# Kernel optimization log

Measured on AMD Instinct MI355X. Metric: run time of the kernel, lower is better.

## Reference

```python
import jax, jax.numpy as jnp
import numpy as np


def _conv1x1(x, w, b):
    # x: (B,C_in,H,W), w: (C_out,C_in), b: (C_out,)
    return jnp.einsum('bchw,oc->bohw', x, w) + b[None, :, None, None]


def _maxpool2x2(x):
    B, C, H, W = x.shape
    return x.reshape(B, C, H // 2, 2, W // 2, 2).max(axis=(3, 5))


def setup_inputs() -> dict:
    key = jax.random.key(0)
    ks = jax.random.split(key, 10)
    B, C, H, W = 16, 64, 64, 64
    d8, d2 = C // 8, C // 2
    s = 0.05
    return {
        'x': jax.random.normal(ks[0], (B, C, H, W), dtype=jnp.float32),
        'w_theta': jax.random.normal(ks[1], (d8, C), dtype=jnp.float32) * s,
        'b_theta': jnp.zeros((d8,), dtype=jnp.float32),
        'w_phi': jax.random.normal(ks[2], (d8, C), dtype=jnp.float32) * s,
        'b_phi': jnp.zeros((d8,), dtype=jnp.float32),
        'w_g': jax.random.normal(ks[3], (d2, C), dtype=jnp.float32) * s,
        'b_g': jnp.zeros((d2,), dtype=jnp.float32),
        'w_o': jax.random.normal(ks[4], (C, d2), dtype=jnp.float32) * s,
        'b_o': jnp.zeros((C,), dtype=jnp.float32),
        'sigma': jnp.ones((1,), dtype=jnp.float32),
    }


def reference(x, w_theta, b_theta, w_phi, b_phi, w_g, b_g, w_o, b_o, sigma):
    B, C, H, W = x.shape
    N = H * W
    theta = _conv1x1(x, w_theta, b_theta).reshape(B, C // 8, N)            # (B, d8, N)
    phi = _maxpool2x2(_conv1x1(x, w_phi, b_phi)).reshape(B, C // 8, N // 4)  # (B, d8, N/4)
    attn = jax.nn.softmax(jnp.einsum('bdn,bdm->bnm', theta, phi), axis=-1)   # (B, N, N/4)
    g = _maxpool2x2(_conv1x1(x, w_g, b_g)).reshape(B, C // 2, N // 4)        # (B, d2, N/4)
    attn_g = jnp.einsum('bcm,bnm->bcn', g, attn).reshape(B, C // 2, H, W)
    attn_g = _conv1x1(attn_g, w_o, b_o)
    return x + sigma[0] * attn_g
```

## Files before the change

kernel.cpp:

```cpp
#include <hip/hip_runtime.h>


#define B_   16
#define C_   64
#define HW_  4096
#define M_   1024

typedef __attribute__((ext_vector_type(8))) short bf16x8;
typedef __attribute__((ext_vector_type(4))) float f32x4;

__device__ __forceinline__ unsigned short f2bf(float f) {
    union { float f; unsigned int u; } v; v.f = f;
    return (unsigned short)((v.u + 0x7FFFu + ((v.u >> 16) & 1u)) >> 16);
}
__device__ __forceinline__ unsigned int pack2(float a, float b) {
    return (unsigned int)f2bf(a) | ((unsigned int)f2bf(b) << 16);
}

__global__ __launch_bounds__(256) void proj_kernel(
    const float* __restrict__ x,
    const float* __restrict__ w_theta, const float* __restrict__ b_theta,
    const float* __restrict__ w_phi,   const float* __restrict__ b_phi,
    const float* __restrict__ w_g,     const float* __restrict__ b_g,
    unsigned short* __restrict__ thetaB,
    unsigned short* __restrict__ phiB32,
    unsigned short* __restrict__ gTp)
{
    __shared__ __align__(16) float x_l[64 * 132];
    __shared__ float pool_l[128][41];

    const int tid = threadIdx.x;
    const int b   = blockIdx.y;
    const int rp  = blockIdx.x;
    const int n0  = rp * 128;

    {
        const float4* src = (const float4*)(x + (size_t)b * C_ * HW_ + n0);
        #pragma unroll
        for (int j = 0; j < 8; j++) {
            int idx = tid + j * 256;
            int c = idx >> 5, p4 = idx & 31;
            float4 v = src[(size_t)c * (HW_ / 4) + p4];
            *(float4*)&x_l[c * 132 + p4 * 4] = v;
        }
    }
    __syncthreads();

    const int px = tid & 127;
    const int og = tid >> 7;

    if (og == 0) {
        float th[8], ph[8], g0[8];
        #pragma unroll
        for (int o = 0; o < 8; o++) { th[o] = b_theta[o]; ph[o] = b_phi[o]; g0[o] = b_g[o]; }
        #pragma unroll 4
        for (int c = 0; c < C_; c++) {
            float xv = x_l[c * 132 + px];
            #pragma unroll
            for (int o = 0; o < 8; o++) th[o] += xv * w_theta[o * 64 + c];
            #pragma unroll
            for (int o = 0; o < 8; o++) ph[o] += xv * w_phi[o * 64 + c];
            #pragma unroll
            for (int o = 0; o < 8; o++) g0[o] += xv * w_g[o * 64 + c];
        }
        unsigned short* tout = thetaB + ((size_t)b * HW_ + n0 + px) * 8;
        uint4 tv;
        tv.x = pack2(th[0], th[1]); tv.y = pack2(th[2], th[3]);
        tv.z = pack2(th[4], th[5]); tv.w = pack2(th[6], th[7]);
        *(uint4*)tout = tv;
        #pragma unroll
        for (int o = 0; o < 8; o++) { pool_l[px][o] = ph[o]; pool_l[px][8 + o] = g0[o]; }
    } else {
        float gg[24];
        #pragma unroll
        for (int o = 0; o < 24; o++) gg[o] = b_g[8 + o];
        #pragma unroll 4
        for (int c = 0; c < C_; c++) {
            float xv = x_l[c * 132 + px];
            #pragma unroll
            for (int o = 0; o < 24; o++) gg[o] += xv * w_g[(8 + o) * 64 + c];
        }
        #pragma unroll
        for (int o = 0; o < 24; o++) pool_l[px][16 + o] = gg[o];
    }
    __syncthreads();

    if (tid < 32) {
        const int pc  = tid;
        const int p00 = 2 * pc, p01 = 2 * pc + 1, p10 = 64 + 2 * pc, p11 = 65 + 2 * pc;
        const int mq  = rp * 32 + pc;
        float o8[8];
        #pragma unroll
        for (int o = 0; o < 8; o++)
            o8[o] = fmaxf(fmaxf(pool_l[p00][o], pool_l[p01][o]),
                          fmaxf(pool_l[p10][o], pool_l[p11][o]));
        unsigned short* pout = phiB32 + ((size_t)b * M_ + mq) * 32;
        uint4 pv;
        pv.x = pack2(o8[0], o8[1]); pv.y = pack2(o8[2], o8[3]);
        pv.z = pack2(o8[4], o8[5]); pv.w = pack2(o8[6], o8[7]);
        ((uint4*)pout)[0] = pv;
        ((uint4*)pout)[1] = make_uint4(0, 0, 0, 0);
        ((uint4*)pout)[2] = make_uint4(0, 0, 0, 0);
        ((uint4*)pout)[3] = make_uint4(0, 0, 0, 0);
    } else if (tid < 64) {
        const int j   = tid - 32;
        const int p00 = 2 * j, p01 = 2 * j + 1, p10 = 64 + 2 * j, p11 = 65 + 2 * j;
        const int pcol = rp * 32 + ((j >> 2) & 3) * 8 + (j >> 4) * 4 + (j & 3);
        unsigned short* gout = gTp + (size_t)b * 32 * M_ + pcol;
        #pragma unroll
        for (int c = 0; c < 32; c++) {
            const int s = c + 8;
            float v = fmaxf(fmaxf(pool_l[p00][s], pool_l[p01][s]),
                            fmaxf(pool_l[p10][s], pool_l[p11][s]));
            gout[(size_t)c * M_] = f2bf(v);
        }
    }
}

__global__ __launch_bounds__(256) void attn_kernel(
    const float* __restrict__ x,
    const unsigned short* __restrict__ thetaB,
    const unsigned short* __restrict__ phiB32,
    const unsigned short* __restrict__ gTp,
    const float* __restrict__ w_o, const float* __restrict__ b_o,
    const float* __restrict__ sigma,
    float* __restrict__ out)
{
    __shared__ float Op_l[4][64 * 33];
    __shared__ float rs_l[4][64];

    const int tid   = threadIdx.x;
    const int b     = blockIdx.y;
    const int qbase = blockIdx.x * 64;
    const int wv    = tid >> 6;
    const int lane  = tid & 63;
    const int ln15  = lane & 15;
    const int quad  = lane >> 4;

    const unsigned short* phiP = phiB32 + (size_t)b * M_ * 32;
    const unsigned short* gP   = gTp    + (size_t)b * 32 * M_;

    bf16x8 th[4];
    {
        const bf16x8 z = {0, 0, 0, 0, 0, 0, 0, 0};
        #pragma unroll
        for (int qt = 0; qt < 4; qt++) {
            const unsigned short* tp =
                thetaB + ((size_t)b * HW_ + qbase + qt * 16 + ln15) * 8;
            bf16x8 t = *(const bf16x8*)tp;
            th[qt] = (quad == 0) ? t : z;
        }
    }

    #define LD_PHI(ch_, mt_) \
        (*(const bf16x8*)(phiP + ((size_t)((ch_) * 64 + (mt_) * 16 + ln15)) * 32 + quad * 8))
    #define LD_G(ch_, h_, s_) \
        (*(const bf16x8*)(gP + (size_t)((h_) * 16 + ln15) * M_ + (ch_) * 64 + (s_) * 32 + quad * 8))

    f32x4 acc[2][4];
    #pragma unroll
    for (int h = 0; h < 2; h++)
        #pragma unroll
        for (int qt = 0; qt < 4; qt++) acc[h][qt] = (f32x4){0.f, 0.f, 0.f, 0.f};
    float rs_p[4] = {0.f, 0.f, 0.f, 0.f};

    bf16x8 pf[4], gf[2][2];
    {
        const int ch = wv * 4;
        #pragma unroll
        for (int mt = 0; mt < 4; mt++) pf[mt] = LD_PHI(ch, mt);
        gf[0][0] = LD_G(ch, 0, 0); gf[0][1] = LD_G(ch, 0, 1);
        gf[1][0] = LD_G(ch, 1, 0); gf[1][1] = LD_G(ch, 1, 1);
    }

    for (int wc = 0; wc < 4; wc++) {
        const int nch = wv * 4 + ((wc < 3) ? wc + 1 : 3);
        bf16x8 npf[4], ngf[2][2];
        #pragma unroll
        for (int mt = 0; mt < 4; mt++) npf[mt] = LD_PHI(nch, mt);
        ngf[0][0] = LD_G(nch, 0, 0); ngf[0][1] = LD_G(nch, 0, 1);
        ngf[1][0] = LD_G(nch, 1, 0); ngf[1][1] = LD_G(nch, 1, 1);

        #pragma unroll
        for (int s = 0; s < 2; s++) {
            #pragma unroll
            for (int qt = 0; qt < 4; qt++) {
                const f32x4 zc = {0.f, 0.f, 0.f, 0.f};
                f32x4 S0 = __builtin_amdgcn_mfma_f32_16x16x32_bf16(pf[2 * s],     th[qt], zc, 0, 0, 0);
                f32x4 S1 = __builtin_amdgcn_mfma_f32_16x16x32_bf16(pf[2 * s + 1], th[qt], zc, 0, 0, 0);
                float e0[4], e1[4];
                #pragma unroll
                for (int r = 0; r < 4; r++) {
                    e0[r] = __expf(S0[r]);
                    e1[r] = __expf(S1[r]);
                    rs_p[qt] += e0[r] + e1[r];
                }
                union { bf16x8 v; unsigned int u[4]; } pb;
                pb.u[0] = pack2(e0[0], e0[1]); pb.u[1] = pack2(e0[2], e0[3]);
                pb.u[2] = pack2(e1[0], e1[1]); pb.u[3] = pack2(e1[2], e1[3]);
                acc[0][qt] = __builtin_amdgcn_mfma_f32_16x16x32_bf16(gf[0][s], pb.v, acc[0][qt], 0, 0, 0);
                acc[1][qt] = __builtin_amdgcn_mfma_f32_16x16x32_bf16(gf[1][s], pb.v, acc[1][qt], 0, 0, 0);
            }
        }

        #pragma unroll
        for (int mt = 0; mt < 4; mt++) pf[mt] = npf[mt];
        gf[0][0] = ngf[0][0]; gf[0][1] = ngf[0][1];
        gf[1][0] = ngf[1][0]; gf[1][1] = ngf[1][1];
    }
    #undef LD_PHI
    #undef LD_G

    {
        float v[4];
        #pragma unroll
        for (int qt = 0; qt < 4; qt++) {
            float t = rs_p[qt];
            t += __shfl_xor(t, 16);
            t += __shfl_xor(t, 32);
            v[qt] = t;
        }
        if (quad == 0) {
            #pragma unroll
            for (int qt = 0; qt < 4; qt++) rs_l[wv][qt * 16 + ln15] = v[qt];
        }
    }
    #pragma unroll
    for (int h = 0; h < 2; h++)
        #pragma unroll
        for (int qt = 0; qt < 4; qt++)
            #pragma unroll
            for (int r = 0; r < 4; r++)
                Op_l[wv][(qt * 16 + ln15) * 33 + h * 16 + quad * 4 + r] = acc[h][qt][r];
    __syncthreads();

    const int q = tid & 63;
    const float rowsum = rs_l[0][q] + rs_l[1][q] + rs_l[2][q] + rs_l[3][q];
    const float sg  = sigma[0];
    const float inv = sg / rowsum;
    float o[32];
    #pragma unroll
    for (int c = 0; c < 32; c++)
        o[c] = Op_l[0][q * 33 + c] + Op_l[1][q * 33 + c]
             + Op_l[2][q * 33 + c] + Op_l[3][q * 33 + c];
    const size_t xb = (size_t)b * C_ * HW_ + qbase + q;
    #pragma unroll
    for (int k = 0; k < 16; k++) {
        const int co = wv * 16 + k;
        float t = 0.f;
        #pragma unroll
        for (int c = 0; c < 32; c++) t += w_o[co * 32 + c] * o[c];
        out[xb + (size_t)co * HW_] = x[xb + (size_t)co * HW_] + t * inv + sg * b_o[co];
    }
}

extern "C" void kernel_launch(void* const* d_in, const int* in_sizes, int n_in,
                              void* d_out, int out_size, void* d_ws, size_t ws_size,
                              hipStream_t stream)
{
    const float* x       = (const float*)d_in[0];
    const float* w_theta = (const float*)d_in[1];
    const float* b_theta = (const float*)d_in[2];
    const float* w_phi   = (const float*)d_in[3];
    const float* b_phi   = (const float*)d_in[4];
    const float* w_g     = (const float*)d_in[5];
    const float* b_g     = (const float*)d_in[6];
    const float* w_o     = (const float*)d_in[7];
    const float* b_o     = (const float*)d_in[8];
    const float* sigma   = (const float*)d_in[9];
    float* out = (float*)d_out;

    unsigned short* thetaB = (unsigned short*)d_ws;
    unsigned short* phiB32 = thetaB + (size_t)B_ * HW_ * 8;
    unsigned short* gTp    = phiB32 + (size_t)B_ * M_ * 32;

    proj_kernel<<<dim3(32, B_), 256, 0, stream>>>(
        x, w_theta, b_theta, w_phi, b_phi, w_g, b_g, thetaB, phiB32, gTp);
    attn_kernel<<<dim3(64, B_), 256, 0, stream>>>(
        x, thetaB, phiB32, gTp, w_o, b_o, sigma, out);
}
```

Measured before the change: 134.4 us.

## Parallelize pool epilogue, truncate bf16 packing, add occupancy hint, drop manual prefetch

In proj_kernel the pooled phi/g write-out is spread across all 256 threads instead of 64, and the zero padding of phiB32 goes out as separate vector stores. In attn_kernel the softmax weights are packed to bf16 by truncation rather than round-to-nearest, which cuts ALU work in the inner loop. The manual double-buffered prefetch of phi/g fragments is replaced by a fully unrolled loop that loads per chunk, and a minimum-blocks launch bound of 4 is added to push occupancy. Truncation adds a small downward bias to the attention weights, and removing the prefetch leaves latency hiding to the compiler and to the extra resident waves.

```diff
diff --git a/kernel.cpp b/kernel.cpp
--- a/kernel.cpp
+++ b/kernel.cpp
@@ -15,6 +15,10 @@
 }
 __device__ __forceinline__ unsigned int pack2(float a, float b) {
     return (unsigned int)f2bf(a) | ((unsigned int)f2bf(b) << 16);
+}
+__device__ __forceinline__ unsigned int pack2t(float a, float b) {
+    union { float f; unsigned int u; } ua, ub; ua.f = a; ub.f = b;
+    return (ua.u >> 16) | (ub.u & 0xFFFF0000u);
 }
 
 __global__ __launch_bounds__(256) void proj_kernel(
@@ -85,39 +89,31 @@
     }
     __syncthreads();
 
-    if (tid < 32) {
-        const int pc  = tid;
-        const int p00 = 2 * pc, p01 = 2 * pc + 1, p10 = 64 + 2 * pc, p11 = 65 + 2 * pc;
-        const int mq  = rp * 32 + pc;
-        float o8[8];
-        #pragma unroll
-        for (int o = 0; o < 8; o++)
-            o8[o] = fmaxf(fmaxf(pool_l[p00][o], pool_l[p01][o]),
-                          fmaxf(pool_l[p10][o], pool_l[p11][o]));
-        unsigned short* pout = phiB32 + ((size_t)b * M_ + mq) * 32;
-        uint4 pv;
-        pv.x = pack2(o8[0], o8[1]); pv.y = pack2(o8[2], o8[3]);
-        pv.z = pack2(o8[4], o8[5]); pv.w = pack2(o8[6], o8[7]);
-        ((uint4*)pout)[0] = pv;
-        ((uint4*)pout)[1] = make_uint4(0, 0, 0, 0);
-        ((uint4*)pout)[2] = make_uint4(0, 0, 0, 0);
-        ((uint4*)pout)[3] = make_uint4(0, 0, 0, 0);
-    } else if (tid < 64) {
-        const int j   = tid - 32;
+    {
+        const int j   = tid & 31;
+        const int grp = tid >> 5;
         const int p00 = 2 * j, p01 = 2 * j + 1, p10 = 64 + 2 * j, p11 = 65 + 2 * j;
+        const int mq   = rp * 32 + j;
         const int pcol = rp * 32 + ((j >> 2) & 3) * 8 + (j >> 4) * 4 + (j & 3);
-        unsigned short* gout = gTp + (size_t)b * 32 * M_ + pcol;
-        #pragma unroll
-        for (int c = 0; c < 32; c++) {
-            const int s = c + 8;
-            float v = fmaxf(fmaxf(pool_l[p00][s], pool_l[p01][s]),
-                            fmaxf(pool_l[p10][s], pool_l[p11][s]));
-            gout[(size_t)c * M_] = f2bf(v);
-        }
-    }
-}
-
-__global__ __launch_bounds__(256) void attn_kernel(
+        #pragma unroll
+        for (int k = 0; k < 5; k++) {
+            const int ch = grp * 5 + k;
+            float v = fmaxf(fmaxf(pool_l[p00][ch], pool_l[p01][ch]),
+                            fmaxf(pool_l[p10][ch], pool_l[p11][ch]));
+            if (ch < 8)
+                phiB32[((size_t)b * M_ + mq) * 32 + ch] = f2bf(v);
+            else
+                gTp[((size_t)b * 32 + (ch - 8)) * M_ + pcol] = f2bf(v);
+        }
+        if (tid < 96) {
+            const int m = tid / 3, seg = tid % 3;
+            *(uint4*)(phiB32 + ((size_t)b * M_ + rp * 32 + m) * 32 + 8 + seg * 8) =
+                make_uint4(0, 0, 0, 0);
+        }
+    }
+}
+
+__global__ __launch_bounds__(256, 4) void attn_kernel(
     const float* __restrict__ x,
     const unsigned short* __restrict__ thetaB,
     const unsigned short* __restrict__ phiB32,
@@ -164,22 +160,15 @@
         for (int qt = 0; qt < 4; qt++) acc[h][qt] = (f32x4){0.f, 0.f, 0.f, 0.f};
     float rs_p[4] = {0.f, 0.f, 0.f, 0.f};
 
-    bf16x8 pf[4], gf[2][2];
-    {
-        const int ch = wv * 4;
+    #pragma unroll
+    for (int wc = 0; wc < 4; wc++) {
+        const int ch = wv * 4 + wc;
+        bf16x8 pf[4];
         #pragma unroll
         for (int mt = 0; mt < 4; mt++) pf[mt] = LD_PHI(ch, mt);
+        bf16x8 gf[2][2];
         gf[0][0] = LD_G(ch, 0, 0); gf[0][1] = LD_G(ch, 0, 1);
         gf[1][0] = LD_G(ch, 1, 0); gf[1][1] = LD_G(ch, 1, 1);
-    }
-
-    for (int wc = 0; wc < 4; wc++) {
-        const int nch = wv * 4 + ((wc < 3) ? wc + 1 : 3);
-        bf16x8 npf[4], ngf[2][2];
-        #pragma unroll
-        for (int mt = 0; mt < 4; mt++) npf[mt] = LD_PHI(nch, mt);
-        ngf[0][0] = LD_G(nch, 0, 0); ngf[0][1] = LD_G(nch, 0, 1);
-        ngf[1][0] = LD_G(nch, 1, 0); ngf[1][1] = LD_G(nch, 1, 1);
 
         #pragma unroll
         for (int s = 0; s < 2; s++) {
@@ -196,17 +185,12 @@
                     rs_p[qt] += e0[r] + e1[r];
                 }
                 union { bf16x8 v; unsigned int u[4]; } pb;
-                pb.u[0] = pack2(e0[0], e0[1]); pb.u[1] = pack2(e0[2], e0[3]);
-                pb.u[2] = pack2(e1[0], e1[1]); pb.u[3] = pack2(e1[2], e1[3]);
+                pb.u[0] = pack2t(e0[0], e0[1]); pb.u[1] = pack2t(e0[2], e0[3]);
+                pb.u[2] = pack2t(e1[0], e1[1]); pb.u[3] = pack2t(e1[2], e1[3]);
                 acc[0][qt] = __builtin_amdgcn_mfma_f32_16x16x32_bf16(gf[0][s], pb.v, acc[0][qt], 0, 0, 0);
                 acc[1][qt] = __builtin_amdgcn_mfma_f32_16x16x32_bf16(gf[1][s], pb.v, acc[1][qt], 0, 0, 0);
             }
         }
-
-        #pragma unroll
-        for (int mt = 0; mt < 4; mt++) pf[mt] = npf[mt];
-        gf[0][0] = ngf[0][0]; gf[0][1] = ngf[0][1];
-        gf[1][0] = ngf[1][0]; gf[1][1] = ngf[1][1];
     }
     #undef LD_PHI
     #undef LD_G
```

Result: faster. 126.8 us (-5.7%).
